# Kernel optimization log

Hardware: AMD Instinct MI355X
Metric: run time of the kernel (lower is better)

The kernel has to match this reference:

```python
import jax, jax.numpy as jnp
import numpy as np

T = 5          # Newton-Schulz iterations
EPS = 1e-05


def reference(X):
    # X: (B, C, L); training-mode IterNorm whitening with num_groups=1
    B, C, L = X.shape
    x = jnp.transpose(X, (1, 0, 2)).reshape(C, -1)        # (d, m)
    d, m = x.shape
    mean = jnp.mean(x, axis=-1, keepdims=True)
    xc = x - mean                                         # (d, m)
    I = jnp.eye(d, dtype=X.dtype)
    Sigma = I * EPS + (xc @ xc.T) * (1.0 / m)             # (d, d)
    rTr = 1.0 / jnp.trace(Sigma)                          # scalar
    Sigma_N = Sigma * rTr
    P = I
    for _ in range(T):
        P = 1.5 * P - 0.5 * (P @ P @ P) @ Sigma_N
    wm = P * jnp.sqrt(rTr)                                # whitening matrix
    xn = wm @ xc                                          # (d, m)
    Xn = jnp.transpose(xn.reshape(C, B, L), (1, 0, 2))
    return Xn


def setup_inputs() -> dict:
    key = jax.random.key(0)
    X = jax.random.normal(key, (32, 64, 8192), dtype=jnp.float32)
    return {"X": X}
```

## Files before the change

### kernel.cpp

```cpp
#include <hip/hip_runtime.h>
#include <math.h>

#define L_DIM   8192
#define NCH     64
#define M_TOT_F 262144.0f
#define EPS_F   1e-5f

typedef float f32x4 __attribute__((ext_vector_type(4)));
typedef short bf16x8 __attribute__((ext_vector_type(8)));

union U8 { unsigned u[4]; bf16x8 v; };

__device__ __forceinline__ void cvt2(float f0, float f1, unsigned& h, unsigned& l) {
    unsigned u0 = __float_as_uint(f0), u1 = __float_as_uint(f1);
    h = (u0 >> 16) | (u1 & 0xFFFF0000u);
    float r0 = f0 - __uint_as_float(u0 & 0xFFFF0000u);
    float r1 = f1 - __uint_as_float(u1 & 0xFFFF0000u);
    l = (__float_as_uint(r0) >> 16) | (__float_as_uint(r1) & 0xFFFF0000u);
}

__device__ __forceinline__ void cvt8(const float* p, bf16x8& hi, bf16x8& lo) {
    float4 f0 = *(const float4*)p;
    float4 f1 = *(const float4*)(p + 4);
    U8 H, L;
    cvt2(f0.x, f0.y, H.u[0], L.u[0]);
    cvt2(f0.z, f0.w, H.u[1], L.u[1]);
    cvt2(f1.x, f1.y, H.u[2], L.u[2]);
    cvt2(f1.z, f1.w, H.u[3], L.u[3]);
    hi = H.v; lo = L.v;
}

__device__ __forceinline__ f32x4 mfma16(bf16x8 a, bf16x8 b, f32x4 c) {
    return __builtin_amdgcn_mfma_f32_16x16x32_bf16(a, b, c, 0, 0, 0);
}

__device__ __forceinline__ f32x4 fzero() {
    f32x4 z; z[0] = 0.f; z[1] = 0.f; z[2] = 0.f; z[3] = 0.f; return z;
}

#define GTPB 8
__global__ __launch_bounds__(256) void gram_kernel(const float* __restrict__ X,
                                                   float* __restrict__ P) {
    __shared__ __align__(16) unsigned short hplane[64 * 72];
    __shared__ __align__(16) unsigned short lplane[64 * 72];
    const int tid  = threadIdx.x;
    const int w    = tid >> 6;
    const int lane = tid & 63;
    const int m    = lane & 15;
    const int q    = lane >> 4;
    const int lrow = tid >> 2;
    const int lq16 = (tid & 3) << 4;

    f32x4 acc1[4], acc2[4];
#pragma unroll
    for (int nb = 0; nb < 4; ++nb) { acc1[nb] = fzero(); acc2[nb] = fzero(); }
    float sacc = 0.f;

    const int tile0 = blockIdx.x * GTPB;
    float4 v[4];
    {
        int t = tile0;
        const float* src = X + ((size_t)((t >> 7) * NCH + lrow)) * L_DIM + ((t & 127) << 6) + lq16;
#pragma unroll
        for (int i = 0; i < 4; ++i) v[i] = ((const float4*)src)[i];
    }

    for (int t = 0; t < GTPB; ++t) {
#pragma unroll
        for (int i = 0; i < 4; ++i) sacc += v[i].x + v[i].y + v[i].z + v[i].w;
        __syncthreads();
#pragma unroll
        for (int i = 0; i < 4; ++i) {
            unsigned h0, l0, h1, l1;
            cvt2(v[i].x, v[i].y, h0, l0);
            cvt2(v[i].z, v[i].w, h1, l1);
            uint2 hh; hh.x = h0; hh.y = h1;
            uint2 ll; ll.x = l0; ll.y = l1;
            *(uint2*)&hplane[lrow * 72 + lq16 + 4 * i] = hh;
            *(uint2*)&lplane[lrow * 72 + lq16 + 4 * i] = ll;
        }
        __syncthreads();
        if (t + 1 < GTPB) {
            int tn = tile0 + t + 1;
            const float* src = X + ((size_t)((tn >> 7) * NCH + lrow)) * L_DIM + ((tn & 127) << 6) + lq16;
#pragma unroll
            for (int i = 0; i < 4; ++i) v[i] = ((const float4*)src)[i];
        }
#pragma unroll
        for (int k0 = 0; k0 < 64; k0 += 32) {
            bf16x8 a = *(const bf16x8*)&hplane[(16 * w + m) * 72 + k0 + 8 * q];
#pragma unroll
            for (int nb = 0; nb < 4; ++nb) {
                bf16x8 bh = *(const bf16x8*)&hplane[(16 * nb + m) * 72 + k0 + 8 * q];
                bf16x8 bl = *(const bf16x8*)&lplane[(16 * nb + m) * 72 + k0 + 8 * q];
                acc1[nb] = mfma16(a, bh, acc1[nb]);
                acc2[nb] = mfma16(a, bl, acc2[nb]);
            }
        }
    }

    float* base = P + (size_t)blockIdx.x * 8256;
#pragma unroll
    for (int nb = 0; nb < 4; ++nb)
#pragma unroll
        for (int r = 0; r < 4; ++r) {
            int grow = 16 * w + 4 * q + r;
            int gcol = 16 * nb + m;
            base[grow * 64 + gcol]        = acc1[nb][r];
            base[4096 + grow * 64 + gcol] = acc2[nb][r];
        }
    sacc += __shfl_xor(sacc, 1);
    sacc += __shfl_xor(sacc, 2);
    if ((tid & 3) == 0) base[8192 + lrow] = sacc;
}

__global__ __launch_bounds__(256) void reduce_kernel(const float* __restrict__ P,
                                                     float* __restrict__ ws) {
    const int tid = threadIdx.x;
    const int w = tid >> 6, lane = tid & 63;
    const int e0 = blockIdx.x * 64;
    float a = 0.f;
#pragma unroll 8
    for (int i = 0; i < 128; ++i)
        a += P[(size_t)(w * 128 + i) * 8256 + e0 + lane];
    __shared__ float red[4][64];
    red[w][lane] = a;
    __syncthreads();
    if (w == 0)
        ws[e0 + lane] = red[0][lane] + red[1][lane] + red[2][lane] + red[3][lane];
}

__device__ __forceinline__ void mm_sym(float* __restrict__ D, const float* __restrict__ A,
                                       const float* __restrict__ B, int w, int m, int q) {
    f32x4 acc[4];
#pragma unroll
    for (int nb = 0; nb < 4; ++nb) acc[nb] = fzero();
#pragma unroll
    for (int k0 = 0; k0 < 64; k0 += 32) {
        bf16x8 ah, al;
        cvt8(&A[(16 * w + m) * 68 + k0 + 8 * q], ah, al);
#pragma unroll
        for (int nb = 0; nb < 4; ++nb) {
            bf16x8 bh, bl;
            cvt8(&B[(16 * nb + m) * 68 + k0 + 8 * q], bh, bl);
            acc[nb] = mfma16(ah, bh, acc[nb]);
            acc[nb] = mfma16(ah, bl, acc[nb]);
            acc[nb] = mfma16(al, bh, acc[nb]);
        }
    }
#pragma unroll
    for (int nb = 0; nb < 4; ++nb)
#pragma unroll
        for (int r = 0; r < 4; ++r)
            D[(16 * w + 4 * q + r) * 68 + 16 * nb + m] = acc[nb][r];
}

__global__ __launch_bounds__(256) void ns_kernel(float* __restrict__ ws) {
    __shared__ __align__(16) float S[64 * 68];
    __shared__ __align__(16) float Pm[64 * 68];
    __shared__ __align__(16) float T1[64 * 68];
    __shared__ __align__(16) float T2[64 * 68];
    __shared__ float mu[64];
    __shared__ float scal[2];

    const int tid = threadIdx.x;
    const int w = tid >> 6, lane = tid & 63;
    const int m = lane & 15, q = lane >> 4;
    const float inv_m = 1.0f / M_TOT_F;

    if (tid < 64) mu[tid] = ws[8192 + tid] * inv_m;
    __syncthreads();

    for (int e = tid; e < 4096; e += 256) {
        int i = e >> 6, j = e & 63;
        float g = (ws[e] + ws[4096 + e] + ws[4096 + (j << 6) + i]) * inv_m;
        S[i * 68 + j]  = g - mu[i] * mu[j] + ((i == j) ? EPS_F : 0.f);
        Pm[i * 68 + j] = (i == j) ? 1.f : 0.f;
    }
    __syncthreads();

    if (tid < 64) {
        float v = S[tid * 68 + tid];
#pragma unroll
        for (int off = 32; off >= 1; off >>= 1) v += __shfl_xor(v, off);
        if (tid == 0) { scal[0] = 1.0f / v; scal[1] = sqrtf(1.0f / v); }
    }
    __syncthreads();
    const float rTr = scal[0];
    for (int e = tid; e < 4096; e += 256) S[(e >> 6) * 68 + (e & 63)] *= rTr;
    __syncthreads();

    for (int it = 0; it < 5; ++it) {
        mm_sym(T1, Pm, Pm, w, m, q);
        __syncthreads();
        mm_sym(T2, T1, Pm, w, m, q);
        __syncthreads();
        f32x4 acc[4];
#pragma unroll
        for (int nb = 0; nb < 4; ++nb) acc[nb] = fzero();
#pragma unroll
        for (int k0 = 0; k0 < 64; k0 += 32) {
            bf16x8 ah, al;
            cvt8(&T2[(16 * w + m) * 68 + k0 + 8 * q], ah, al);
#pragma unroll
            for (int nb = 0; nb < 4; ++nb) {
                bf16x8 bh, bl;
                cvt8(&S[(16 * nb + m) * 68 + k0 + 8 * q], bh, bl);
                acc[nb] = mfma16(ah, bh, acc[nb]);
                acc[nb] = mfma16(ah, bl, acc[nb]);
                acc[nb] = mfma16(al, bh, acc[nb]);
            }
        }
#pragma unroll
        for (int nb = 0; nb < 4; ++nb)
#pragma unroll
            for (int r = 0; r < 4; ++r) {
                int idx = (16 * w + 4 * q + r) * 68 + 16 * nb + m;
                Pm[idx] = 1.5f * Pm[idx] - 0.5f * acc[nb][r];
            }
        __syncthreads();
    }

    const float s = scal[1];
    unsigned short* hp = (unsigned short*)ws;
    unsigned short* lp = hp + 4096;
    for (int e = tid; e < 4096; e += 256) {
        int i = e >> 6, j = e & 63;
        float v = Pm[i * 68 + j] * s;
        unsigned u = __float_as_uint(v);
        hp[e] = (unsigned short)(u >> 16);
        float r = v - __uint_as_float(u & 0xFFFF0000u);
        lp[e] = (unsigned short)(__float_as_uint(r) >> 16);
    }
    if (tid < 64) {
        float a = 0.f;
#pragma unroll 8
        for (int k = 0; k < 64; ++k) a += Pm[tid * 68 + k] * mu[k];
        ws[8256 + tid] = -a * s;
    }
}

#define ATPB 4
__global__ __launch_bounds__(256) void apply_kernel(const float* __restrict__ X,
                                                    float* __restrict__ Y,
                                                    const float* __restrict__ ws) {
    const int tid  = threadIdx.x;
    const int w    = tid >> 6;
    const int lane = tid & 63;
    const int m    = lane & 15;
    const int q    = lane >> 4;

    const unsigned short* hp = (const unsigned short*)ws;
    const unsigned short* lp = hp + 4096;

    bf16x8 Ah[2], Al[2];
#pragma unroll
    for (int kk = 0; kk < 2; ++kk) {
        Ah[kk] = *(const bf16x8*)&hp[(16 * w + m) * 64 + 32 * kk + 8 * q];
        Al[kk] = *(const bf16x8*)&lp[(16 * w + m) * 64 + 32 * kk + 8 * q];
    }
    const float4 bias4 = *(const float4*)&ws[8256 + 16 * w + 4 * q];

    for (int t = 0; t < ATPB; ++t) {
        int tile = blockIdx.x * ATPB + t;
        int bidx = tile >> 7;
        int l0   = (tile & 127) << 6;
        const float* xb = X + (size_t)bidx * NCH * L_DIM + l0;

        f32x4 acc[4];
#pragma unroll
        for (int nb = 0; nb < 4; ++nb) {
            acc[nb][0] = bias4.x; acc[nb][1] = bias4.y;
            acc[nb][2] = bias4.z; acc[nb][3] = bias4.w;
        }
#pragma unroll
        for (int k0 = 0; k0 < 64; k0 += 32) {
            const int kk = k0 >> 5;
#pragma unroll
            for (int nb = 0; nb < 4; ++nb) {
                float f[8];
#pragma unroll
                for (int j = 0; j < 8; ++j)
                    f[j] = xb[(size_t)(k0 + 8 * q + j) * L_DIM + 16 * nb + m];
                U8 H, L;
                cvt2(f[0], f[1], H.u[0], L.u[0]);
                cvt2(f[2], f[3], H.u[1], L.u[1]);
                cvt2(f[4], f[5], H.u[2], L.u[2]);
                cvt2(f[6], f[7], H.u[3], L.u[3]);
                acc[nb] = mfma16(Ah[kk], H.v, acc[nb]);
                acc[nb] = mfma16(Ah[kk], L.v, acc[nb]);
                acc[nb] = mfma16(Al[kk], H.v, acc[nb]);
            }
        }
#pragma unroll
        for (int nb = 0; nb < 4; ++nb)
#pragma unroll
            for (int r = 0; r < 4; ++r)
                Y[((size_t)bidx * NCH + 16 * w + 4 * q + r) * L_DIM + l0 + 16 * nb + m] = acc[nb][r];
    }
}

extern "C" void kernel_launch(void* const* d_in, const int* in_sizes, int n_in,
                              void* d_out, int out_size, void* d_ws, size_t ws_size,
                              hipStream_t stream) {
    const float* X = (const float*)d_in[0];
    float* Y  = (float*)d_out;
    float* ws = (float*)d_ws;
    float* scratch = (float*)d_out;

    hipLaunchKernelGGL(gram_kernel,   dim3(512),  dim3(256), 0, stream, X, scratch);
    hipLaunchKernelGGL(reduce_kernel, dim3(129),  dim3(256), 0, stream, scratch, ws);
    hipLaunchKernelGGL(ns_kernel,     dim3(1),    dim3(256), 0, stream, ws);
    hipLaunchKernelGGL(apply_kernel,  dim3(1024), dim3(256), 0, stream, X, Y, ws);
}
```

Measured before the change: 167.6 us.

## Stage X tiles through swizzled LDS with register prefetch in apply kernel

The apply kernel now loads each 64x64 X tile with coalesced float4 global loads and converts it to bf16 hi/lo planes once per block. The planes go into an XOR-swizzled shared-memory layout, replacing the previous per-wave strided scalar loads, where every wave re-read and re-converted the whole tile. The next tile is prefetched into registers while MFMAs run on the current one. This is meant to cut redundant global traffic and conversion work, at the cost of two __syncthreads per tile, 16KB of LDS, and extra registers.

```diff
diff --git a/kernel.cpp b/kernel.cpp
--- a/kernel.cpp
+++ b/kernel.cpp
@@ -244,15 +244,18 @@
 __global__ __launch_bounds__(256) void apply_kernel(const float* __restrict__ X,
                                                     float* __restrict__ Y,
                                                     const float* __restrict__ ws) {
+    __shared__ __align__(16) unsigned short hplane[4096];
+    __shared__ __align__(16) unsigned short lplane[4096];
     const int tid  = threadIdx.x;
     const int w    = tid >> 6;
     const int lane = tid & 63;
     const int m    = lane & 15;
     const int q    = lane >> 4;
+    const int cp   = tid & 31;
+    const int lg   = tid >> 5;
 
     const unsigned short* hp = (const unsigned short*)ws;
     const unsigned short* lp = hp + 4096;
-
     bf16x8 Ah[2], Al[2];
 #pragma unroll
     for (int kk = 0; kk < 2; ++kk) {
@@ -260,12 +263,55 @@
         Al[kk] = *(const bf16x8*)&lp[(16 * w + m) * 64 + 32 * kk + 8 * q];
     }
     const float4 bias4 = *(const float4*)&ws[8256 + 16 * w + 4 * q];
+
+    unsigned* hw = (unsigned*)hplane;
+    unsigned* lw = (unsigned*)lplane;
+
+    float4 va[2], vb[2];
+    {
+        int tile = blockIdx.x * ATPB;
+        const float* xb = X + (size_t)(tile >> 7) * (NCH * L_DIM) + ((tile & 127) << 6)
+                          + (size_t)(2 * cp) * L_DIM + 4 * lg;
+#pragma unroll
+        for (int s = 0; s < 2; ++s) {
+            va[s] = *(const float4*)(xb + 32 * s);
+            vb[s] = *(const float4*)(xb + 32 * s + L_DIM);
+        }
+    }
 
     for (int t = 0; t < ATPB; ++t) {
         int tile = blockIdx.x * ATPB + t;
         int bidx = tile >> 7;
         int l0   = (tile & 127) << 6;
-        const float* xb = X + (size_t)bidx * NCH * L_DIM + l0;
+
+        __syncthreads();
+#pragma unroll
+        for (int s = 0; s < 2; ++s) {
+            float fa[4], fb[4];
+            *(float4*)fa = va[s];
+            *(float4*)fb = vb[s];
+#pragma unroll
+            for (int i = 0; i < 4; ++i) {
+                int l = 4 * lg + 32 * s + i;
+                unsigned h, lo2;
+                cvt2(fa[i], fb[i], h, lo2);
+                int widx = l * 32 + (((cp >> 2) ^ (l & 7)) << 2) + (cp & 3);
+                hw[widx] = h;
+                lw[widx] = lo2;
+            }
+        }
+        __syncthreads();
+
+        if (t + 1 < ATPB) {
+            int tn = tile + 1;
+            const float* xb = X + (size_t)(tn >> 7) * (NCH * L_DIM) + ((tn & 127) << 6)
+                              + (size_t)(2 * cp) * L_DIM + 4 * lg;
+#pragma unroll
+            for (int s = 0; s < 2; ++s) {
+                va[s] = *(const float4*)(xb + 32 * s);
+                vb[s] = *(const float4*)(xb + 32 * s + L_DIM);
+            }
+        }
 
         f32x4 acc[4];
 #pragma unroll
@@ -274,29 +320,23 @@
             acc[nb][2] = bias4.z; acc[nb][3] = bias4.w;
         }
 #pragma unroll
-        for (int k0 = 0; k0 < 64; k0 += 32) {
-            const int kk = k0 >> 5;
+        for (int kk = 0; kk < 2; ++kk)
 #pragma unroll
             for (int nb = 0; nb < 4; ++nb) {
-                float f[8];
-#pragma unroll
-                for (int j = 0; j < 8; ++j)
-                    f[j] = xb[(size_t)(k0 + 8 * q + j) * L_DIM + 16 * nb + m];
-                U8 H, L;
-                cvt2(f[0], f[1], H.u[0], L.u[0]);
-                cvt2(f[2], f[3], H.u[1], L.u[1]);
-                cvt2(f[4], f[5], H.u[2], L.u[2]);
-                cvt2(f[6], f[7], H.u[3], L.u[3]);
-                acc[nb] = mfma16(Ah[kk], H.v, acc[nb]);
-                acc[nb] = mfma16(Ah[kk], L.v, acc[nb]);
-                acc[nb] = mfma16(Al[kk], H.v, acc[nb]);
-            }
-        }
+                int l = 16 * nb + m;
+                int saddr = l * 64 + ((((4 * kk + q) ^ (l & 7))) << 3);
+                bf16x8 bh = *(const bf16x8*)&hplane[saddr];
+                bf16x8 bl = *(const bf16x8*)&lplane[saddr];
+                acc[nb] = mfma16(Ah[kk], bh, acc[nb]);
+                acc[nb] = mfma16(Ah[kk], bl, acc[nb]);
+                acc[nb] = mfma16(Al[kk], bh, acc[nb]);
+            }
+
 #pragma unroll
         for (int nb = 0; nb < 4; ++nb)
 #pragma unroll
-            for (int r = 0; r < 4; ++r)
-                Y[((size_t)bidx * NCH + 16 * w + 4 * q + r) * L_DIM + l0 + 16 * nb + m] = acc[nb][r];
+            for (int rr = 0; rr < 4; ++rr)
+                Y[((size_t)bidx * NCH + 16 * w + 4 * q + rr) * L_DIM + l0 + 16 * nb + m] = acc[nb][rr];
     }
 }
 
```

Measured after the change: 157.2 us. 1.07x faster.
